# Kernel tuning notes

Measured on AMD Instinct MI355X. Metric: run time of the kernel, lower is better.

Reference implementation:

```python
import jax, jax.numpy as jnp
import numpy as np

HIDDEN = 1024

def setup_inputs() -> dict:
    key = jax.random.key(0)
    ks = jax.random.split(key, 4)
    scale = 1.0 / np.sqrt(HIDDEN)
    return {
        "X": jax.random.normal(ks[0], (4, 4096, HIDDEN), dtype=jnp.float32),
        "Wq": jax.random.normal(ks[1], (HIDDEN, HIDDEN), dtype=jnp.float32) * scale,
        "bq": jnp.zeros((HIDDEN,), dtype=jnp.float32),
        "Wk": jax.random.normal(ks[2], (HIDDEN, HIDDEN), dtype=jnp.float32) * scale,
        "bk": jnp.zeros((HIDDEN,), dtype=jnp.float32),
        "Wv": jax.random.normal(ks[3], (HIDDEN, HIDDEN), dtype=jnp.float32) * scale,
        "bv": jnp.zeros((HIDDEN,), dtype=jnp.float32),
    }

def reference(X, Wq, bq, Wk, bk, Wv, bv):
    # nn.Linear: x @ W.T + b
    Q = jnp.einsum("bsh,dh->bsd", X, Wq) + bq   # [B,S,H]
    K = jnp.einsum("bsh,dh->bsd", X, Wk) + bk
    V = jnp.einsum("bsh,dh->bsd", X, Wv) + bv
    scores = jnp.einsum("bsd,btd->bst", Q, K) / jnp.sqrt(jnp.asarray(X.shape[-1], X.dtype))  # [B,S,S]
    attn = jax.nn.softmax(scores, axis=-1)
    return jnp.einsum("bst,btd->bsd", attn, V)  # [B,S,H]
```

## Files before the change

### kernel.cpp

```cpp
#include <hip/hip_runtime.h>
#include <math.h>

#define HIDDEN 1024
#define SEQ    4096
#define BATCH  4

typedef _Float16 f16x8 __attribute__((ext_vector_type(8)));
typedef float    floatx4 __attribute__((ext_vector_type(4)));

__device__ inline void gld16(const void* g, void* l) {
    __builtin_amdgcn_global_load_lds(
        (const __attribute__((address_space(1))) unsigned int*)g,
        (__attribute__((address_space(3))) unsigned int*)l, 16, 0, 0);
}

template<int MODE>
__global__ __launch_bounds__(256)
void gemm128_kernel(const _Float16* __restrict__ A,
                    const _Float16* __restrict__ Bq,
                    const _Float16* __restrict__ Bk,
                    const _Float16* __restrict__ Bv,
                    const float* __restrict__ bq,
                    const float* __restrict__ bk,
                    const float* __restrict__ bv,
                    float alpha,
                    _Float16* __restrict__ Eo,
                    _Float16* __restrict__ Qo,
                    _Float16* __restrict__ Ko,
                    _Float16* __restrict__ Vo,
                    float* __restrict__ Lsum,
                    int K, int lda, int ldb) {
    __shared__ __align__(16) char smem[16384];
    char* sA = smem;
    char* sB = smem + 8192;

    const int tid  = threadIdx.x;
    const int lane = tid & 63;
    const int w    = tid >> 6;
    const int wm   = w & 1;
    const int wn   = w >> 1;
    const int quad = lane >> 4;
    const int l16  = lane & 15;
    const int swz  = (l16 >> 1) & 3;

    int row0, col0;
    if (MODE == 5) {
        const int n    = blockIdx.x + 24 * blockIdx.y;
        const int xcd  = n & 7;
        const int slot = n >> 3;
        const int cc   = slot % 24;
        const int rg   = xcd + 8 * (slot / 24);
        row0 = rg * 128;
        col0 = cc * 128;
    } else {
        row0 = blockIdx.y * 128;
        col0 = blockIdx.x * 128;
    }
    const int bz = blockIdx.z;

    if (MODE == 3) {
        A    += (size_t)bz * SEQ * HIDDEN;
        Bq   += (size_t)bz * SEQ * HIDDEN;
        Eo   += (size_t)bz * SEQ * SEQ;
        Lsum += (size_t)bz * SEQ;
    }

    const _Float16* Bsrc = Bq;
    int colbase = col0;
    int which = 0;
    if (MODE == 5) {
        which = col0 >> 10;
        Bsrc = (which == 0) ? Bq : (which == 1) ? Bk : Bv;
        colbase = col0 & 1023;
    }

    floatx4 acc[4][4];
    #pragma unroll
    for (int i = 0; i < 4; ++i)
        #pragma unroll
        for (int j = 0; j < 4; ++j) acc[i][j] = (floatx4){0.f, 0.f, 0.f, 0.f};

    const f16x8* pA = (const f16x8*)sA;
    const f16x8* pB = (const f16x8*)sB;

    int srow[2], scol[2];
    #pragma unroll
    for (int it = 0; it < 2; ++it) {
        const int n = tid + it * 256;
        srow[it] = n >> 2;
        scol[it] = (n & 3) ^ ((srow[it] >> 1) & 3);
    }

    for (int k0 = 0; k0 < K; k0 += 32) {
        #pragma unroll
        for (int it = 0; it < 2; ++it) {
            const int n = tid + it * 256;
            const size_t ga = (size_t)(row0 + srow[it]) * lda + (size_t)k0 + scol[it] * 8;
            const size_t gb = (size_t)(colbase + srow[it]) * ldb + (size_t)k0 + scol[it] * 8;
            gld16(A + ga, sA + n * 16);
            gld16(Bsrc + gb, sB + n * 16);
        }
        __syncthreads();

        f16x8 af[4];
        #pragma unroll
        for (int i = 0; i < 4; ++i) {
            const int r = wm * 64 + i * 16 + l16;
            af[i] = pA[r * 4 + (quad ^ swz)];
        }
        #pragma unroll
        for (int j = 0; j < 4; ++j) {
            const int c = wn * 64 + j * 16 + l16;
            const f16x8 bf = pB[c * 4 + (quad ^ swz)];
            #pragma unroll
            for (int i = 0; i < 4; ++i)
                acc[i][j] = __builtin_amdgcn_mfma_f32_16x16x32_f16(af[i], bf, acc[i][j], 0, 0, 0);
        }
        __syncthreads();
    }

    #pragma unroll
    for (int i = 0; i < 4; ++i) {
        const int r0 = row0 + wm * 64 + i * 16 + quad * 4;
        float rp[4] = {0.f, 0.f, 0.f, 0.f};

        #pragma unroll
        for (int j = 0; j < 4; ++j) {
            const int cl = (MODE == 5 ? colbase : col0) + wn * 64 + j * 16 + l16;

            if (MODE == 5) {
                const float bcol = (which == 0 ? bq : which == 1 ? bk : bv)[cl];
                if (which < 2) {
                    _Float16* O = (which == 0) ? Qo : Ko;
                    #pragma unroll
                    for (int reg = 0; reg < 4; ++reg)
                        O[(size_t)(r0 + reg) * HIDDEN + cl] =
                            (_Float16)(acc[i][j][reg] + bcol);
                } else {
                    const int bb = r0 >> 12;
                    const int s  = r0 & 4095;
                    _Float16 t[4];
                    #pragma unroll
                    for (int reg = 0; reg < 4; ++reg)
                        t[reg] = (_Float16)(acc[i][j][reg] + bcol);
                    *(uint2*)&Vo[((size_t)bb * HIDDEN + cl) * SEQ + s] = *(const uint2*)t;
                }
            } else {
                #pragma unroll
                for (int reg = 0; reg < 4; ++reg) {
                    const float v = exp2f(alpha * acc[i][j][reg] - 5.770780163555856f);
                    const _Float16 vh = (_Float16)v;
                    Eo[(size_t)(r0 + reg) * SEQ + cl] = vh;
                    rp[reg] += (float)vh;
                }
            }
        }

        if (MODE == 3) {
            #pragma unroll
            for (int off = 1; off < 16; off <<= 1)
                #pragma unroll
                for (int reg = 0; reg < 4; ++reg)
                    rp[reg] += __shfl_xor(rp[reg], off, 64);
            if (l16 == 0)
                #pragma unroll
                for (int reg = 0; reg < 4; ++reg)
                    atomicAdd(&Lsum[r0 + reg], rp[reg]);
        }
    }
}

__global__ __launch_bounds__(512, 2)
void qk8_kernel(const _Float16* __restrict__ Q,
                const _Float16* __restrict__ Kmat,
                _Float16* __restrict__ E,
                float* __restrict__ Lsum,
                float alpha) {
    __shared__ __align__(16) char smem[131072];
    char* sA = smem;
    char* sB = smem + 65536;

    const int tid  = threadIdx.x;
    const int lane = tid & 63;
    const int w    = tid >> 6;
    const int wm   = w & 1;
    const int wn   = w >> 1;
    const int quad = lane >> 4;
    const int l16  = lane & 15;
    const int swz  = (l16 >> 1) & 3;

    const int bx   = blockIdx.x;
    const int z    = blockIdx.y;
    const int wgid = (bx & 7) * 32 + (bx >> 3);
    const int row0 = (wgid >> 4) * 256;
    const int col0 = (wgid & 15) * 256;

    const _Float16* Abase = Q    + (size_t)z * SEQ * HIDDEN + (size_t)row0 * HIDDEN;
    const _Float16* Bbase = Kmat + (size_t)z * SEQ * HIDDEN + (size_t)col0 * HIDDEN;
    E    += (size_t)z * SEQ * SEQ;
    Lsum += (size_t)z * SEQ;

    const int n0 = tid, n1 = tid + 512;
    const int r0s = n0 >> 2, p0s = n0 & 3;
    const int r1s = n1 >> 2, p1s = n1 & 3;
    const int off0 = r0s * HIDDEN + (p0s ^ ((r0s >> 1) & 3)) * 8;
    const int off1 = r1s * HIDDEN + (p1s ^ ((r1s >> 1) & 3)) * 8;

    auto stage = [&](const _Float16* base, char* lh, int kt, int kh) {
        const int kb = kt * 64 + kh * 32;
        gld16(base + off0 + kb, lh + n0 * 16);
        gld16(base + off1 + kb, lh + n1 * 16);
    };

    floatx4 acc[8][4];
    #pragma unroll
    for (int i = 0; i < 8; ++i)
        #pragma unroll
        for (int j = 0; j < 4; ++j) acc[i][j] = (floatx4){0.f, 0.f, 0.f, 0.f};

    f16x8 afA[4], afB[4], bfX[4], bfY[4];

#define RD_AF(DST, RH, KH, B_)                                                \
  { const f16x8* pAh = (const f16x8*)(sA + ((B_) * 2 + (KH)) * 16384);        \
    _Pragma("unroll")                                                         \
    for (int i = 0; i < 4; ++i)                                               \
      DST[i] = pAh[(wm * 128 + (RH) * 64 + i * 16 + l16) * 4 + (quad ^ swz)]; }

#define RD_BF(DST, KH, B_)                                                    \
  { const f16x8* pBh = (const f16x8*)(sB + ((B_) * 2 + (KH)) * 16384);        \
    _Pragma("unroll")                                                         \
    for (int j = 0; j < 4; ++j)                                               \
      DST[j] = pBh[(wn * 64 + j * 16 + l16) * 4 + (quad ^ swz)]; }

#define MM(RH, AF, BF)                                                        \
  __builtin_amdgcn_sched_barrier(0);                                          \
  __builtin_amdgcn_s_setprio(1);                                              \
  _Pragma("unroll")                                                           \
  for (int j = 0; j < 4; ++j)                                                 \
    _Pragma("unroll")                                                         \
    for (int i = 0; i < 4; ++i)                                               \
      acc[(RH) * 4 + i][j] = __builtin_amdgcn_mfma_f32_16x16x32_f16(          \
          AF[i], BF[j], acc[(RH) * 4 + i][j], 0, 0, 0);                       \
  __builtin_amdgcn_s_setprio(0);

#define QK_TILE(T_, S01, S23, W0S, W2S, RDNEXT)                               \
  { const int b_ = (T_) & 1, nb_ = b_ ^ 1;                                    \
                                                            \
    __builtin_amdgcn_s_barrier();                                             \
    RD_AF(afB, 1, 0, b_);                                                     \
    if (S01) stage(Abase, sA + (nb_ * 2 + 1) * 16384, (T_) + 1, 1);           \
    MM(0, afA, bfX)                                                           \
    asm volatile("s_waitcnt vmcnt(" W0S ")" ::: "memory");                    \
                                                            \
    __builtin_amdgcn_s_barrier();                                             \
    RD_AF(afA, 0, 1, b_);                                                     \
    RD_BF(bfY, 1, b_);                                                        \
    if (S01) stage(Bbase, sB + (nb_ * 2 + 1) * 16384, (T_) + 1, 1);           \
    MM(1, afB, bfX)                                                           \
                                                            \
    __builtin_amdgcn_s_barrier();                                             \
    RD_AF(afB, 1, 1, b_);                                                     \
    if (S23) stage(Abase, sA + (b_ * 2 + 0) * 16384, (T_) + 2, 0);            \
    MM(0, afA, bfY)                                                           \
    if (RDNEXT) asm volatile("s_waitcnt vmcnt(" W2S ")" ::: "memory");        \
                                                            \
    __builtin_amdgcn_s_barrier();                                             \
    if (RDNEXT) {                                                             \
      RD_AF(afA, 0, 0, nb_);                                                  \
      RD_BF(bfX, 0, nb_);                                                     \
    }                                                                         \
    if (S23) stage(Bbase, sB + (b_ * 2 + 0) * 16384, (T_) + 2, 0);            \
    MM(1, afB, bfY)                                                           \
  }

    stage(Abase, sA + 0 * 16384, 0, 0);
    stage(Bbase, sB + 0 * 16384, 0, 0);
    stage(Abase, sA + 1 * 16384, 0, 1);
    stage(Bbase, sB + 1 * 16384, 0, 1);
    stage(Abase, sA + 2 * 16384, 1, 0);
    stage(Bbase, sB + 2 * 16384, 1, 0);
    asm volatile("s_waitcnt vmcnt(8)" ::: "memory");
    __builtin_amdgcn_s_barrier();
    RD_AF(afA, 0, 0, 0);
    RD_BF(bfX, 0, 0);

    for (int t = 0; t < 14; ++t) QK_TILE(t, 1, 1, "6", "6", 1)
    QK_TILE(14, 1, 0, "6", "4", 1)
    QK_TILE(15, 0, 0, "0", "0", 0)

#undef QK_TILE
#undef MM
#undef RD_BF
#undef RD_AF

    #pragma unroll
    for (int i = 0; i < 8; ++i) {
        const int r0 = row0 + wm * 128 + i * 16 + quad * 4;
        float rp[4] = {0.f, 0.f, 0.f, 0.f};
        #pragma unroll
        for (int j = 0; j < 4; ++j) {
            const int cl = col0 + wn * 64 + j * 16 + l16;
            #pragma unroll
            for (int reg = 0; reg < 4; ++reg) {
                const float v = exp2f(alpha * acc[i][j][reg] - 5.770780163555856f);
                const _Float16 vh = (_Float16)v;
                E[(size_t)(r0 + reg) * SEQ + cl] = vh;
                rp[reg] += (float)vh;
            }
        }
        #pragma unroll
        for (int off = 1; off < 16; off <<= 1)
            #pragma unroll
            for (int reg = 0; reg < 4; ++reg)
                rp[reg] += __shfl_xor(rp[reg], off, 64);
        if (l16 == 0)
            #pragma unroll
            for (int reg = 0; reg < 4; ++reg)
                atomicAdd(&Lsum[r0 + reg], rp[reg]);
    }
}

__global__ __launch_bounds__(256, 2)
void gemm_pv_kernel(const _Float16* __restrict__ A,
                    const _Float16* __restrict__ B,
                    float* __restrict__ Cf,
                    const float* __restrict__ Lsum) {
    __shared__ __align__(16) char smem[24576];
    char* sA = smem;
    char* sB = smem + 8192;

    const int tid  = threadIdx.x;
    const int lane = tid & 63;
    const int w    = tid >> 6;
    const int wm   = w & 1;
    const int wn   = w >> 1;
    const int quad = lane >> 4;
    const int l16  = lane & 15;
    const int swz  = (l16 >> 1) & 3;

    const int n    = blockIdx.x;
    const int xcd  = n & 7;
    const int slot = n >> 3;
    const int c    = slot & 3;
    const int rg   = xcd + 8 * (slot >> 2);
    const int r    = rg & 31;
    const int bz   = rg >> 5;

    const int row0 = r * 128;
    const int col0 = c * 256;

    A    += (size_t)bz * SEQ * SEQ;
    B    += (size_t)bz * HIDDEN * SEQ;
    Cf   += (size_t)bz * SEQ * HIDDEN;
    Lsum += (size_t)bz * SEQ;

    floatx4 acc[4][8];
    #pragma unroll
    for (int i = 0; i < 4; ++i)
        #pragma unroll
        for (int j = 0; j < 8; ++j) acc[i][j] = (floatx4){0.f, 0.f, 0.f, 0.f};

    const f16x8* pA = (const f16x8*)sA;
    const f16x8* pB = (const f16x8*)sB;

    for (int k0 = 0; k0 < SEQ; k0 += 32) {
        #pragma unroll
        for (int it = 0; it < 2; ++it) {
            const int nc = tid + it * 256;
            const int sr = nc >> 2;
            const int sc = (nc & 3) ^ ((sr >> 1) & 3);
            gld16(A + (size_t)(row0 + sr) * SEQ + k0 + sc * 8, sA + nc * 16);
        }
        #pragma unroll
        for (int it = 0; it < 4; ++it) {
            const int nc = tid + it * 256;
            const int sr = nc >> 2;
            const int sc = (nc & 3) ^ ((sr >> 1) & 3);
            gld16(B + (size_t)(col0 + sr) * SEQ + k0 + sc * 8, sB + nc * 16);
        }
        __syncthreads();

        f16x8 af[4];
        #pragma unroll
        for (int i = 0; i < 4; ++i) {
            const int rr = wm * 64 + i * 16 + l16;
            af[i] = pA[rr * 4 + (quad ^ swz)];
        }
        #pragma unroll
        for (int j = 0; j < 8; ++j) {
            const int cc = wn * 128 + j * 16 + l16;
            const f16x8 bf = pB[cc * 4 + (quad ^ swz)];
            #pragma unroll
            for (int i = 0; i < 4; ++i)
                acc[i][j] = __builtin_amdgcn_mfma_f32_16x16x32_f16(af[i], bf, acc[i][j], 0, 0, 0);
        }
        __syncthreads();
    }

    #pragma unroll
    for (int i = 0; i < 4; ++i) {
        const int r0 = row0 + wm * 64 + i * 16 + quad * 4;
        float linv[4];
        #pragma unroll
        for (int reg = 0; reg < 4; ++reg) linv[reg] = 1.0f / Lsum[r0 + reg];
        #pragma unroll
        for (int j = 0; j < 8; ++j) {
            const int cl = col0 + wn * 128 + j * 16 + l16;
            #pragma unroll
            for (int reg = 0; reg < 4; ++reg)
                Cf[(size_t)(r0 + reg) * HIDDEN + cl] = acc[i][j][reg] * linv[reg];
        }
    }
}

__global__ __launch_bounds__(256)
void cast_x_kernel(const float* __restrict__ in, _Float16* __restrict__ out) {
    const int i = blockIdx.x * 256 + threadIdx.x;
    const float4 x = ((const float4*)in)[i];
    _Float16 h[4] = {(_Float16)x.x, (_Float16)x.y, (_Float16)x.z, (_Float16)x.w};
    ((uint2*)out)[i] = *(const uint2*)h;
}

__global__ __launch_bounds__(256)
void cast_w_kernel(const float* __restrict__ w0, const float* __restrict__ w1,
                   const float* __restrict__ w2,
                   _Float16* __restrict__ o0, _Float16* __restrict__ o1,
                   _Float16* __restrict__ o2) {
    const float* in = (blockIdx.z == 0) ? w0 : (blockIdx.z == 1) ? w1 : w2;
    _Float16* out   = (blockIdx.z == 0) ? o0 : (blockIdx.z == 1) ? o1 : o2;
    const int i = blockIdx.x * 256 + threadIdx.x;
    const float4 x = ((const float4*)in)[i];
    _Float16 h[4] = {(_Float16)x.x, (_Float16)x.y, (_Float16)x.z, (_Float16)x.w};
    ((uint2*)out)[i] = *(const uint2*)h;
}

extern "C" void kernel_launch(void* const* d_in, const int* in_sizes, int n_in,
                              void* d_out, int out_size, void* d_ws, size_t ws_size,
                              hipStream_t stream) {
    const float* X  = (const float*)d_in[0];
    const float* Wq = (const float*)d_in[1];
    const float* bq = (const float*)d_in[2];
    const float* Wk = (const float*)d_in[3];
    const float* bk = (const float*)d_in[4];
    const float* Wv = (const float*)d_in[5];
    const float* bv = (const float*)d_in[6];
    float* out = (float*)d_out;

    char* ws = (char*)d_ws;
    const size_t EB = (size_t)BATCH * SEQ * SEQ * 2;
    const size_t XB = (size_t)BATCH * SEQ * HIDDEN * 2;
    const size_t WB = (size_t)HIDDEN * HIDDEN * 2;

    _Float16* E   = (_Float16*)ws;
    _Float16* Xh  = (_Float16*)ws;
    _Float16* Wqh = (_Float16*)(ws + XB);
    _Float16* Wkh = (_Float16*)(ws + XB + WB);
    _Float16* Wvh = (_Float16*)(ws + XB + 2 * WB);
    _Float16* Qh  = (_Float16*)(ws + EB);
    _Float16* Kh  = (_Float16*)(ws + EB + XB);
    _Float16* Vt  = (_Float16*)(ws + EB + 2 * XB);
    float*    Lsum= (float*)   (ws + EB + 3 * XB);

    cast_x_kernel<<<dim3(16384), dim3(256), 0, stream>>>(X, Xh);
    cast_w_kernel<<<dim3(1024, 1, 3), dim3(256), 0, stream>>>(
        Wq, Wk, Wv, Wqh, Wkh, Wvh);

    hipMemsetAsync(Lsum, 0, (size_t)BATCH * SEQ * sizeof(float), stream);

    gemm128_kernel<5><<<dim3(24, 128, 1), dim3(256), 0, stream>>>(
        Xh, Wqh, Wkh, Wvh, bq, bk, bv, 1.0f,
        nullptr, Qh, Kh, Vt, nullptr,
        HIDDEN, HIDDEN, HIDDEN);

    const float alpha2 = (1.0f / 32.0f) * 1.4426950408889634f;
    qk8_kernel<<<dim3(256, 4), dim3(512), 0, stream>>>(Qh, Kh, E, Lsum, alpha2);

    gemm_pv_kernel<<<dim3(512), dim3(256), 0, stream>>>(E, Vt, out, Lsum);
}
```

Baseline: 597.1 us.

## Unify QKV projection, QK and PV GEMMs onto pipelined 256x256 tile kernel

Replaces the simple 128-tile QKV projection kernel and the single-buffered PV kernel with one templated 256x256-tile, 512-thread kernel that reuses the software-pipelined, double-buffered main loop of the QK kernel. The template parameter selects the epilogue (bias plus Q/K/V store, exp plus row-sum atomics, or normalise and store) and the number of K tiles. The intent is to give the projection and PV GEMMs the higher data reuse and latency hiding of the pipelined kernel. In exchange each block uses 128 KB of LDS and the grids are smaller (768 and 256 blocks), which may reduce occupancy and load balance. There is also a new 'unroll 2' on the tile loop.

```diff
diff --git a/kernel.cpp b/kernel.cpp
--- a/kernel.cpp
+++ b/kernel.cpp
@@ -14,9 +14,9 @@
         (__attribute__((address_space(3))) unsigned int*)l, 16, 0, 0);
 }
 
-template<int MODE>
-__global__ __launch_bounds__(256)
-void gemm128_kernel(const _Float16* __restrict__ A,
+template<int MODE, int NT>
+__global__ __launch_bounds__(512)
+void gemm256_kernel(const _Float16* __restrict__ A,
                     const _Float16* __restrict__ Bq,
                     const _Float16* __restrict__ Bk,
                     const _Float16* __restrict__ Bv,
@@ -28,11 +28,12 @@
                     _Float16* __restrict__ Qo,
                     _Float16* __restrict__ Ko,
                     _Float16* __restrict__ Vo,
-                    float* __restrict__ Lsum,
-                    int K, int lda, int ldb) {
-    __shared__ __align__(16) char smem[16384];
+                    float* __restrict__ Cf,
+                    float* __restrict__ Lsum) {
+    constexpr int LDAB = (MODE == 4) ? SEQ : HIDDEN;
+    __shared__ __align__(16) char smem[131072];
     char* sA = smem;
-    char* sB = smem + 8192;
+    char* sB = smem + 65536;
 
     const int tid  = threadIdx.x;
     const int lane = tid & 63;
@@ -43,168 +44,47 @@
     const int l16  = lane & 15;
     const int swz  = (l16 >> 1) & 3;
 
-    int row0, col0;
-    if (MODE == 5) {
-        const int n    = blockIdx.x + 24 * blockIdx.y;
-        const int xcd  = n & 7;
-        const int slot = n >> 3;
-        const int cc   = slot % 24;
-        const int rg   = xcd + 8 * (slot / 24);
-        row0 = rg * 128;
-        col0 = cc * 128;
+    int row0, col0, z = 0;
+    if constexpr (MODE == 5) {
+        const int n = blockIdx.x, xcd = n & 7, slot = n >> 3;
+        const int cc = slot % 12, rg = xcd + 8 * (slot / 12);
+        row0 = rg * 256; col0 = cc * 256;
+    } else if constexpr (MODE == 3) {
+        z = blockIdx.y;
+        const int bx = blockIdx.x, wgid = (bx & 7) * 32 + (bx >> 3);
+        row0 = (wgid >> 4) * 256; col0 = (wgid & 15) * 256;
     } else {
-        row0 = blockIdx.y * 128;
-        col0 = blockIdx.x * 128;
+        z = blockIdx.y;
+        const int n = blockIdx.x, xcd = n & 7, slot = n >> 3;
+        const int cc = slot & 3, rg = xcd + 8 * (slot >> 2);
+        row0 = rg * 256; col0 = cc * 256;
     }
-    const int bz = blockIdx.z;
-
-    if (MODE == 3) {
-        A    += (size_t)bz * SEQ * HIDDEN;
-        Bq   += (size_t)bz * SEQ * HIDDEN;
-        Eo   += (size_t)bz * SEQ * SEQ;
-        Lsum += (size_t)bz * SEQ;
+
+    const _Float16* Abase;
+    const _Float16* Bbase;
+    int colbase = col0, which = 0;
+    if constexpr (MODE == 5) {
+        which = col0 >> 10; colbase = col0 & 1023;
+        const _Float16* Bsrc = (which == 0) ? Bq : (which == 1) ? Bk : Bv;
+        Abase = A + (size_t)row0 * HIDDEN;
+        Bbase = Bsrc + (size_t)colbase * HIDDEN;
+    } else if constexpr (MODE == 3) {
+        Abase = A  + (size_t)z * SEQ * HIDDEN + (size_t)row0 * HIDDEN;
+        Bbase = Bq + (size_t)z * SEQ * HIDDEN + (size_t)col0 * HIDDEN;
+        Eo   += (size_t)z * SEQ * SEQ;
+        Lsum += (size_t)z * SEQ;
+    } else {
+        Abase = A  + (size_t)z * SEQ * SEQ    + (size_t)row0 * SEQ;
+        Bbase = Bq + (size_t)z * HIDDEN * SEQ + (size_t)col0 * SEQ;
+        Cf   += (size_t)z * SEQ * HIDDEN;
+        Lsum += (size_t)z * SEQ;
     }
-
-    const _Float16* Bsrc = Bq;
-    int colbase = col0;
-    int which = 0;
-    if (MODE == 5) {
-        which = col0 >> 10;
-        Bsrc = (which == 0) ? Bq : (which == 1) ? Bk : Bv;
-        colbase = col0 & 1023;
-    }
-
-    floatx4 acc[4][4];
-    #pragma unroll
-    for (int i = 0; i < 4; ++i)
-        #pragma unroll
-        for (int j = 0; j < 4; ++j) acc[i][j] = (floatx4){0.f, 0.f, 0.f, 0.f};
-
-    const f16x8* pA = (const f16x8*)sA;
-    const f16x8* pB = (const f16x8*)sB;
-
-    int srow[2], scol[2];
-    #pragma unroll
-    for (int it = 0; it < 2; ++it) {
-        const int n = tid + it * 256;
-        srow[it] = n >> 2;
-        scol[it] = (n & 3) ^ ((srow[it] >> 1) & 3);
-    }
-
-    for (int k0 = 0; k0 < K; k0 += 32) {
-        #pragma unroll
-        for (int it = 0; it < 2; ++it) {
-            const int n = tid + it * 256;
-            const size_t ga = (size_t)(row0 + srow[it]) * lda + (size_t)k0 + scol[it] * 8;
-            const size_t gb = (size_t)(colbase + srow[it]) * ldb + (size_t)k0 + scol[it] * 8;
-            gld16(A + ga, sA + n * 16);
-            gld16(Bsrc + gb, sB + n * 16);
-        }
-        __syncthreads();
-
-        f16x8 af[4];
-        #pragma unroll
-        for (int i = 0; i < 4; ++i) {
-            const int r = wm * 64 + i * 16 + l16;
-            af[i] = pA[r * 4 + (quad ^ swz)];
-        }
-        #pragma unroll
-        for (int j = 0; j < 4; ++j) {
-            const int c = wn * 64 + j * 16 + l16;
-            const f16x8 bf = pB[c * 4 + (quad ^ swz)];
-            #pragma unroll
-            for (int i = 0; i < 4; ++i)
-                acc[i][j] = __builtin_amdgcn_mfma_f32_16x16x32_f16(af[i], bf, acc[i][j], 0, 0, 0);
-        }
-        __syncthreads();
-    }
-
-    #pragma unroll
-    for (int i = 0; i < 4; ++i) {
-        const int r0 = row0 + wm * 64 + i * 16 + quad * 4;
-        float rp[4] = {0.f, 0.f, 0.f, 0.f};
-
-        #pragma unroll
-        for (int j = 0; j < 4; ++j) {
-            const int cl = (MODE == 5 ? colbase : col0) + wn * 64 + j * 16 + l16;
-
-            if (MODE == 5) {
-                const float bcol = (which == 0 ? bq : which == 1 ? bk : bv)[cl];
-                if (which < 2) {
-                    _Float16* O = (which == 0) ? Qo : Ko;
-                    #pragma unroll
-                    for (int reg = 0; reg < 4; ++reg)
-                        O[(size_t)(r0 + reg) * HIDDEN + cl] =
-                            (_Float16)(acc[i][j][reg] + bcol);
-                } else {
-                    const int bb = r0 >> 12;
-                    const int s  = r0 & 4095;
-                    _Float16 t[4];
-                    #pragma unroll
-                    for (int reg = 0; reg < 4; ++reg)
-                        t[reg] = (_Float16)(acc[i][j][reg] + bcol);
-                    *(uint2*)&Vo[((size_t)bb * HIDDEN + cl) * SEQ + s] = *(const uint2*)t;
-                }
-            } else {
-                #pragma unroll
-                for (int reg = 0; reg < 4; ++reg) {
-                    const float v = exp2f(alpha * acc[i][j][reg] - 5.770780163555856f);
-                    const _Float16 vh = (_Float16)v;
-                    Eo[(size_t)(r0 + reg) * SEQ + cl] = vh;
-                    rp[reg] += (float)vh;
-                }
-            }
-        }
-
-        if (MODE == 3) {
-            #pragma unroll
-            for (int off = 1; off < 16; off <<= 1)
-                #pragma unroll
-                for (int reg = 0; reg < 4; ++reg)
-                    rp[reg] += __shfl_xor(rp[reg], off, 64);
-            if (l16 == 0)
-                #pragma unroll
-                for (int reg = 0; reg < 4; ++reg)
-                    atomicAdd(&Lsum[r0 + reg], rp[reg]);
-        }
-    }
-}
-
-__global__ __launch_bounds__(512, 2)
-void qk8_kernel(const _Float16* __restrict__ Q,
-                const _Float16* __restrict__ Kmat,
-                _Float16* __restrict__ E,
-                float* __restrict__ Lsum,
-                float alpha) {
-    __shared__ __align__(16) char smem[131072];
-    char* sA = smem;
-    char* sB = smem + 65536;
-
-    const int tid  = threadIdx.x;
-    const int lane = tid & 63;
-    const int w    = tid >> 6;
-    const int wm   = w & 1;
-    const int wn   = w >> 1;
-    const int quad = lane >> 4;
-    const int l16  = lane & 15;
-    const int swz  = (l16 >> 1) & 3;
-
-    const int bx   = blockIdx.x;
-    const int z    = blockIdx.y;
-    const int wgid = (bx & 7) * 32 + (bx >> 3);
-    const int row0 = (wgid >> 4) * 256;
-    const int col0 = (wgid & 15) * 256;
-
-    const _Float16* Abase = Q    + (size_t)z * SEQ * HIDDEN + (size_t)row0 * HIDDEN;
-    const _Float16* Bbase = Kmat + (size_t)z * SEQ * HIDDEN + (size_t)col0 * HIDDEN;
-    E    += (size_t)z * SEQ * SEQ;
-    Lsum += (size_t)z * SEQ;
 
     const int n0 = tid, n1 = tid + 512;
     const int r0s = n0 >> 2, p0s = n0 & 3;
     const int r1s = n1 >> 2, p1s = n1 & 3;
-    const int off0 = r0s * HIDDEN + (p0s ^ ((r0s >> 1) & 3)) * 8;
-    const int off1 = r1s * HIDDEN + (p1s ^ ((r1s >> 1) & 3)) * 8;
+    const int off0 = r0s * LDAB + (p0s ^ ((r0s >> 1) & 3)) * 8;
+    const int off1 = r1s * LDAB + (p1s ^ ((r1s >> 1) & 3)) * 8;
 
     auto stage = [&](const _Float16* base, char* lh, int kt, int kh) {
         const int kb = kt * 64 + kh * 32;
@@ -284,9 +164,10 @@
     RD_AF(afA, 0, 0, 0);
     RD_BF(bfX, 0, 0);
 
-    for (int t = 0; t < 14; ++t) QK_TILE(t, 1, 1, "6", "6", 1)
-    QK_TILE(14, 1, 0, "6", "4", 1)
-    QK_TILE(15, 0, 0, "0", "0", 0)
+    #pragma unroll 2
+    for (int t = 0; t < NT - 2; ++t) QK_TILE(t, 1, 1, "6", "6", 1)
+    QK_TILE(NT - 2, 1, 0, "6", "4", 1)
+    QK_TILE(NT - 1, 0, 0, "0", "0", 0)
 
 #undef QK_TILE
 #undef MM
@@ -296,119 +177,60 @@
     #pragma unroll
     for (int i = 0; i < 8; ++i) {
         const int r0 = row0 + wm * 128 + i * 16 + quad * 4;
-        float rp[4] = {0.f, 0.f, 0.f, 0.f};
-        #pragma unroll
-        for (int j = 0; j < 4; ++j) {
-            const int cl = col0 + wn * 64 + j * 16 + l16;
-            #pragma unroll
-            for (int reg = 0; reg < 4; ++reg) {
-                const float v = exp2f(alpha * acc[i][j][reg] - 5.770780163555856f);
-                const _Float16 vh = (_Float16)v;
-                E[(size_t)(r0 + reg) * SEQ + cl] = vh;
-                rp[reg] += (float)vh;
+        if constexpr (MODE == 3) {
+            float rp[4] = {0.f, 0.f, 0.f, 0.f};
+            #pragma unroll
+            for (int j = 0; j < 4; ++j) {
+                const int cl = col0 + wn * 64 + j * 16 + l16;
+                #pragma unroll
+                for (int reg = 0; reg < 4; ++reg) {
+                    const float v = exp2f(alpha * acc[i][j][reg] - 5.770780163555856f);
+                    const _Float16 vh = (_Float16)v;
+                    Eo[(size_t)(r0 + reg) * SEQ + cl] = vh;
+                    rp[reg] += (float)vh;
+                }
             }
-        }
-        #pragma unroll
-        for (int off = 1; off < 16; off <<= 1)
-            #pragma unroll
-            for (int reg = 0; reg < 4; ++reg)
-                rp[reg] += __shfl_xor(rp[reg], off, 64);
-        if (l16 == 0)
-            #pragma unroll
-            for (int reg = 0; reg < 4; ++reg)
-                atomicAdd(&Lsum[r0 + reg], rp[reg]);
-    }
-}
-
-__global__ __launch_bounds__(256, 2)
-void gemm_pv_kernel(const _Float16* __restrict__ A,
-                    const _Float16* __restrict__ B,
-                    float* __restrict__ Cf,
-                    const float* __restrict__ Lsum) {
-    __shared__ __align__(16) char smem[24576];
-    char* sA = smem;
-    char* sB = smem + 8192;
-
-    const int tid  = threadIdx.x;
-    const int lane = tid & 63;
-    const int w    = tid >> 6;
-    const int wm   = w & 1;
-    const int wn   = w >> 1;
-    const int quad = lane >> 4;
-    const int l16  = lane & 15;
-    const int swz  = (l16 >> 1) & 3;
-
-    const int n    = blockIdx.x;
-    const int xcd  = n & 7;
-    const int slot = n >> 3;
-    const int c    = slot & 3;
-    const int rg   = xcd + 8 * (slot >> 2);
-    const int r    = rg & 31;
-    const int bz   = rg >> 5;
-
-    const int row0 = r * 128;
-    const int col0 = c * 256;
-
-    A    += (size_t)bz * SEQ * SEQ;
-    B    += (size_t)bz * HIDDEN * SEQ;
-    Cf   += (size_t)bz * SEQ * HIDDEN;
-    Lsum += (size_t)bz * SEQ;
-
-    floatx4 acc[4][8];
-    #pragma unroll
-    for (int i = 0; i < 4; ++i)
-        #pragma unroll
-        for (int j = 0; j < 8; ++j) acc[i][j] = (floatx4){0.f, 0.f, 0.f, 0.f};
-
-    const f16x8* pA = (const f16x8*)sA;
-    const f16x8* pB = (const f16x8*)sB;
-
-    for (int k0 = 0; k0 < SEQ; k0 += 32) {
-        #pragma unroll
-        for (int it = 0; it < 2; ++it) {
-            const int nc = tid + it * 256;
-            const int sr = nc >> 2;
-            const int sc = (nc & 3) ^ ((sr >> 1) & 3);
-            gld16(A + (size_t)(row0 + sr) * SEQ + k0 + sc * 8, sA + nc * 16);
-        }
-        #pragma unroll
-        for (int it = 0; it < 4; ++it) {
-            const int nc = tid + it * 256;
-            const int sr = nc >> 2;
-            const int sc = (nc & 3) ^ ((sr >> 1) & 3);
-            gld16(B + (size_t)(col0 + sr) * SEQ + k0 + sc * 8, sB + nc * 16);
-        }
-        __syncthreads();
-
-        f16x8 af[4];
-        #pragma unroll
-        for (int i = 0; i < 4; ++i) {
-            const int rr = wm * 64 + i * 16 + l16;
-            af[i] = pA[rr * 4 + (quad ^ swz)];
-        }
-        #pragma unroll
-        for (int j = 0; j < 8; ++j) {
-            const int cc = wn * 128 + j * 16 + l16;
-            const f16x8 bf = pB[cc * 4 + (quad ^ swz)];
-            #pragma unroll
-            for (int i = 0; i < 4; ++i)
-                acc[i][j] = __builtin_amdgcn_mfma_f32_16x16x32_f16(af[i], bf, acc[i][j], 0, 0, 0);
-        }
-        __syncthreads();
-    }
-
-    #pragma unroll
-    for (int i = 0; i < 4; ++i) {
-        const int r0 = row0 + wm * 64 + i * 16 + quad * 4;
-        float linv[4];
-        #pragma unroll
-        for (int reg = 0; reg < 4; ++reg) linv[reg] = 1.0f / Lsum[r0 + reg];
-        #pragma unroll
-        for (int j = 0; j < 8; ++j) {
-            const int cl = col0 + wn * 128 + j * 16 + l16;
-            #pragma unroll
-            for (int reg = 0; reg < 4; ++reg)
-                Cf[(size_t)(r0 + reg) * HIDDEN + cl] = acc[i][j][reg] * linv[reg];
+            #pragma unroll
+            for (int off = 1; off < 16; off <<= 1)
+                #pragma unroll
+                for (int reg = 0; reg < 4; ++reg)
+                    rp[reg] += __shfl_xor(rp[reg], off, 64);
+            if (l16 == 0)
+                #pragma unroll
+                for (int reg = 0; reg < 4; ++reg)
+                    atomicAdd(&Lsum[r0 + reg], rp[reg]);
+        } else if constexpr (MODE == 5) {
+            #pragma unroll
+            for (int j = 0; j < 4; ++j) {
+                const int cl = colbase + wn * 64 + j * 16 + l16;
+                const float bcol = (which == 0 ? bq : which == 1 ? bk : bv)[cl];
+                if (which < 2) {
+                    _Float16* O = (which == 0) ? Qo : Ko;
+                    #pragma unroll
+                    for (int reg = 0; reg < 4; ++reg)
+                        O[(size_t)(r0 + reg) * HIDDEN + cl] =
+                            (_Float16)(acc[i][j][reg] + bcol);
+                } else {
+                    const int bb = r0 >> 12;
+                    const int s  = r0 & 4095;
+                    _Float16 tq[4];
+                    #pragma unroll
+                    for (int reg = 0; reg < 4; ++reg)
+                        tq[reg] = (_Float16)(acc[i][j][reg] + bcol);
+                    *(uint2*)&Vo[((size_t)bb * HIDDEN + cl) * SEQ + s] = *(const uint2*)tq;
+                }
+            }
+        } else {
+            float linv[4];
+            #pragma unroll
+            for (int reg = 0; reg < 4; ++reg) linv[reg] = 1.0f / Lsum[r0 + reg];
+            #pragma unroll
+            for (int j = 0; j < 4; ++j) {
+                const int cl = col0 + wn * 64 + j * 16 + l16;
+                #pragma unroll
+                for (int reg = 0; reg < 4; ++reg)
+                    Cf[(size_t)(r0 + reg) * HIDDEN + cl] = acc[i][j][reg] * linv[reg];
+            }
         }
     }
 }
@@ -467,13 +289,16 @@
 
     hipMemsetAsync(Lsum, 0, (size_t)BATCH * SEQ * sizeof(float), stream);
 
-    gemm128_kernel<5><<<dim3(24, 128, 1), dim3(256), 0, stream>>>(
-        Xh, Wqh, Wkh, Wvh, bq, bk, bv, 1.0f,
-        nullptr, Qh, Kh, Vt, nullptr,
-        HIDDEN, HIDDEN, HIDDEN);
+    gemm256_kernel<5, 16><<<dim3(768), dim3(512), 0, stream>>>(
+        Xh, Wqh, Wkh, Wvh, bq, bk, bv, 0.f,
+        nullptr, Qh, Kh, Vt, nullptr, nullptr);
 
     const float alpha2 = (1.0f / 32.0f) * 1.4426950408889634f;
-    qk8_kernel<<<dim3(256, 4), dim3(512), 0, stream>>>(Qh, Kh, E, Lsum, alpha2);
-
-    gemm_pv_kernel<<<dim3(512), dim3(256), 0, stream>>>(E, Vt, out, Lsum);
-}
+    gemm256_kernel<3, 16><<<dim3(256, 4), dim3(512), 0, stream>>>(
+        Qh, Kh, nullptr, nullptr, nullptr, nullptr, nullptr, alpha2,
+        E, nullptr, nullptr, nullptr, nullptr, Lsum);
+
+    gemm256_kernel<4, 64><<<dim3(64, 4), dim3(512), 0, stream>>>(
+        E, Vt, nullptr, nullptr, nullptr, nullptr, nullptr, 0.f,
+        nullptr, nullptr, nullptr, nullptr, out, Lsum);
+}
```

Result: faster. 527.0 us (-11.7%).
